# Kernel optimization log

Hardware: AMD Instinct MI355X
Metric: run time of the kernel (lower is better)

## Reference

```python
import jax, jax.numpy as jnp
import numpy as np

B, H, W, C = 64, 224, 224, 3
P = 16
DIM = 768
DEPTH = 12
NH, DH = 12, 64
FF = 3072
NPATCH = (H // P) * (W // P)   # 196
L = NPATCH + 1                 # 197 tokens (CLS + patches)
KEEP = int(L * (1.0 - 0.75))   # 49 unmasked tokens


def setup_inputs() -> dict:
    key = jax.random.key(0)
    ks = jax.random.split(key, 16)
    s = 0.02
    inp = {
        'inputs': jax.random.normal(ks[0], (B, H, W, C), jnp.float32),
        'conv_w': jax.random.normal(ks[1], (P, P, C, DIM), jnp.float32) * s,
        'ct':     jax.random.normal(ks[2], (1, 1, DIM), jnp.float32) * s,
        'pe':     jax.random.normal(ks[3], (1, L, DIM), jnp.float32) * s,
        'ln1_s': jnp.ones((DEPTH, DIM), jnp.float32),
        'ln1_b': jnp.zeros((DEPTH, DIM), jnp.float32),
        'qkv_w': jax.random.normal(ks[4], (DEPTH, DIM, 3 * NH * DH), jnp.float32) * s,
        'proj_w': jax.random.normal(ks[5], (DEPTH, NH * DH, DIM), jnp.float32) * s,
        'ln2_s': jnp.ones((DEPTH, DIM), jnp.float32),
        'ln2_b': jnp.zeros((DEPTH, DIM), jnp.float32),
        'w1': jax.random.normal(ks[6], (DEPTH, DIM, FF), jnp.float32) * s,
        'b1': jnp.zeros((DEPTH, FF), jnp.float32),
        'w2': jax.random.normal(ks[7], (DEPTH, FF, DIM), jnp.float32) * s,
        'b2': jnp.zeros((DEPTH, DIM), jnp.float32),
        # Faithful to original: permutation of arange(1, L+1); max value 197
        # is out-of-range and gets clamped by JAX gather, exactly as upstream.
        'mask_idx': jax.random.permutation(ks[8], jnp.arange(1, L + 1))[:KEEP].astype(jnp.int32),
    }
    return inp


def _layernorm(x, scale, bias, eps=1e-9):
    m = jnp.mean(x, axis=-1, keepdims=True)
    v = jnp.var(x, axis=-1, keepdims=True)
    return (x - m) * jax.lax.rsqrt(v + eps) * scale + bias


def _encoder(x, layer_params):
    # x: [B, KEEP, DIM]; layer_params leaves stacked on axis 0 (DEPTH)
    inv_sqrt_d = 1.0 / jnp.sqrt(jnp.float32(DH))

    def block(x, p):
        ln1s, ln1b, qw, pw, ln2s, ln2b, w1, b1, w2, b2 = p
        h = _layernorm(x, ln1s, ln1b)
        qkv = h @ qw                                   # [B, Lk, 3*NH*DH]
        q, k, v = jnp.split(qkv, 3, axis=-1)
        def heads(t):
            return t.reshape(x.shape[0], -1, NH, DH).transpose(0, 2, 1, 3)
        q, k, v = heads(q), heads(k), heads(v)         # [B, NH, Lk, DH]
        att = jax.nn.softmax(jnp.einsum('bhqd,bhkd->bhqk', q, k) * inv_sqrt_d)
        o = jnp.einsum('bhqk,bhkd->bhqd', att, v)
        o = o.transpose(0, 2, 1, 3).reshape(x.shape[0], -1, NH * DH) @ pw
        x = x + o
        h2 = _layernorm(x, ln2s, ln2b)
        x = x + (jax.nn.gelu(h2 @ w1 + b1) @ w2 + b2)
        return x, None

    x, _ = jax.lax.scan(block, x, layer_params)
    return x


def reference(inputs, conv_w, ct, pe, ln1_s, ln1_b, qkv_w, proj_w,
              ln2_s, ln2_b, w1, b1, w2, b2, mask_idx):
    # patch embed: stride-P conv, no bias
    out = jax.lax.conv_general_dilated(
        inputs, conv_w, window_strides=(P, P), padding='VALID',
        dimension_numbers=('NHWC', 'HWIO', 'NHWC'))      # [B, 14, 14, DIM]
    out = out.reshape(out.shape[0], -1, out.shape[3])     # [B, 196, DIM]
    out = jnp.concatenate((jnp.repeat(ct, out.shape[0], axis=0), out), axis=1)
    out = out + pe                                        # [B, 197, DIM]
    patches = out[:, mask_idx]                            # [B, 49, DIM]
    layer_params = (ln1_s, ln1_b, qkv_w, proj_w, ln2_s, ln2_b, w1, b1, w2, b2)
    return _encoder(patches, layer_params)
```

## Files before the change

### kernel.cpp

```cpp
#include <hip/hip_runtime.h>
#include <hip/hip_bf16.h>
#include <math.h>

#define DIMV   768
#define BATCH  64
#define KEEPT  49
#define MTOK   (BATCH*KEEPT)
#define NHEADS 12
#define DHEAD  64
#define FFV    3072
#define NDEPTH 12

typedef short short8 __attribute__((ext_vector_type(8)));
typedef float floatx4 __attribute__((ext_vector_type(4)));
typedef unsigned short ushort;
typedef unsigned short ushortx8 __attribute__((ext_vector_type(8)));

__device__ __forceinline__ ushort f2bf(float f) {
  __hip_bfloat16 h = __float2bfloat16(f);
  return *(ushort*)&h;
}

__device__ __forceinline__ void async_cp16(const void* g, void* l) {
  __builtin_amdgcn_global_load_lds((const __attribute__((address_space(1))) void*)g,
                                   (__attribute__((address_space(3))) void*)l,
                                   16, 0, 0);
}

__global__ __launch_bounds__(256) void gather_patches(
    const float* __restrict__ inp, const int* __restrict__ mask,
    __hip_bfloat16* __restrict__ apix)
{
  int gid = blockIdx.x * 256 + threadIdx.x;
  if (gid >= MTOK * DIMV) return;
  int r = gid / DIMV, k = gid - r * DIMV;
  int b = r / KEEPT, t = r - b * KEEPT;
  int j = mask[t];
  j = j < 0 ? 0 : (j > 196 ? 196 : j);
  float v = 0.f;
  if (j > 0) {
    int p  = j - 1, py = p / 14, px = p - py * 14;
    int ky = k / 48, rem = k - ky * 48, kx = rem / 3, c = rem - kx * 3;
    v = inp[(((b * 224) + py * 16 + ky) * 224 + px * 16 + kx) * 3 + c];
  }
  apix[gid] = __float2bfloat16(v);
}

__global__ __launch_bounds__(256) void layernorm_k(
    const float* __restrict__ x, const float* __restrict__ sc,
    const float* __restrict__ bi, __hip_bfloat16* __restrict__ out)
{
  __shared__ float red[8];
  int r = blockIdx.x;
  const float* xr = x + (size_t)r * DIMV;
  int t = threadIdx.x;
  float v[3];
  float s = 0.f, ss = 0.f;
#pragma unroll
  for (int i = 0; i < 3; i++) {
    float a = xr[t + i * 256];
    v[i] = a; s += a; ss += a * a;
  }
#pragma unroll
  for (int off = 32; off > 0; off >>= 1) {
    s  += __shfl_down(s,  off, 64);
    ss += __shfl_down(ss, off, 64);
  }
  int wave = t >> 6, lane = t & 63;
  if (lane == 0) { red[wave] = s; red[4 + wave] = ss; }
  __syncthreads();
  if (t == 0) {
    float a  = red[0] + red[1] + red[2] + red[3];
    float b2 = red[4] + red[5] + red[6] + red[7];
    float m  = a * (1.f / DIMV);
    float var = b2 * (1.f / DIMV) - m * m;
    red[0] = m;
    red[1] = rsqrtf(var + 1e-9f);
  }
  __syncthreads();
  float m = red[0], rs = red[1];
  __hip_bfloat16* outr = out + (size_t)r * DIMV;
#pragma unroll
  for (int i = 0; i < 3; i++) {
    int d = t + i * 256;
    outr[d] = __float2bfloat16((v[i] - m) * rs * sc[d] + bi[d]);
  }
}

__device__ __forceinline__ void transpose_tile64(
    const float* __restrict__ src, __hip_bfloat16* __restrict__ dst,
    int R, int C, int tr, int tcc)
{
  __shared__ float lds[64][65];
  const int tid = threadIdx.x;
  const int r0 = tr * 64, c0 = tcc * 64;
  const int lr = tid >> 4, lc4 = (tid & 15) * 4;
#pragma unroll
  for (int p = 0; p < 4; p++) {
    float4 v = *(const float4*)(src + (size_t)(r0 + p * 16 + lr) * C + c0 + lc4);
    lds[p * 16 + lr][lc4 + 0] = v.x;
    lds[p * 16 + lr][lc4 + 1] = v.y;
    lds[p * 16 + lr][lc4 + 2] = v.z;
    lds[p * 16 + lr][lc4 + 3] = v.w;
  }
  __syncthreads();
  const int c = tid >> 2, rc = (tid & 3) * 8;
  ushortx8 o0, o1;
#pragma unroll
  for (int j = 0; j < 8; j++) o0[j] = f2bf(lds[rc + j][c]);
#pragma unroll
  for (int j = 0; j < 8; j++) o1[j] = f2bf(lds[rc + 32 + j][c]);
  ushort* drow = (ushort*)dst + (size_t)(c0 + c) * R + r0;
  *(ushortx8*)(drow + rc)      = o0;
  *(ushortx8*)(drow + rc + 32) = o1;
}

__global__ __launch_bounds__(256) void transpose_one(
    const float* __restrict__ src, __hip_bfloat16* __restrict__ dst, int R, int C)
{
  int tc = C >> 6;
  transpose_tile64(src, dst, R, C, blockIdx.x / tc, blockIdx.x % tc);
}

#define QKV_TE  ((size_t)2304*768)
#define PROJ_TE ((size_t)768*768)
#define W1_TE   ((size_t)3072*768)
#define W2_TE   ((size_t)768*3072)
#define LSTRIDE (QKV_TE + PROJ_TE + W1_TE + W2_TE)

__global__ __launch_bounds__(256) void convert_weights(
    const float* __restrict__ qkv_w, const float* __restrict__ proj_w,
    const float* __restrict__ w1, const float* __restrict__ w2,
    __hip_bfloat16* __restrict__ dstBase, int layer0, size_t dstStride)
{
  int l = layer0 + blockIdx.y;
  __hip_bfloat16* d = dstBase + (size_t)blockIdx.y * dstStride;
  int tile = blockIdx.x;
  const float* src; __hip_bfloat16* dst; int R, C, t0;
  if (tile < 432)       { src = qkv_w  + (size_t)l*768*2304; dst = d;                          R=768;  C=2304; t0=tile; }
  else if (tile < 576)  { src = proj_w + (size_t)l*768*768;  dst = d + QKV_TE;                 R=768;  C=768;  t0=tile-432; }
  else if (tile < 1152) { src = w1     + (size_t)l*768*3072; dst = d + QKV_TE+PROJ_TE;         R=768;  C=3072; t0=tile-576; }
  else                  { src = w2     + (size_t)l*3072*768; dst = d + QKV_TE+PROJ_TE+W1_TE;   R=3072; C=768;  t0=tile-1152; }
  int tc = C >> 6;
  transpose_tile64(src, dst, R, C, t0 / tc, t0 % tc);
}

enum { EPI_NONE = 0, EPI_RESID = 1, EPI_BIAS_GELU = 2, EPI_BIAS_RESID = 3,
       EPI_EMBED = 4 };

template <int EPI, bool OUT_BF16>
__global__ __launch_bounds__(256) void gemm_mfma(
    const ushort* __restrict__ A, const ushort* __restrict__ Bt,
    const float* __restrict__ Cin, const float* __restrict__ bias,
    const float* __restrict__ pe, const int* __restrict__ mask,
    void* __restrict__ Cout, int M, int N, int K)
{
  __shared__ ushort As[2][128 * 64];
  __shared__ ushort Bs[2][64 * 64];

  const int tid  = threadIdx.x;
  const int wave = tid >> 6, lane = tid & 63;
  const int bm = blockIdx.y, bn = blockIdx.x;
  const int fr = lane & 15, fc = lane >> 4;

  floatx4 acc[2][4];
#pragma unroll
  for (int i = 0; i < 2; i++)
#pragma unroll
    for (int j = 0; j < 4; j++) { floatx4 z = {0.f,0.f,0.f,0.f}; acc[i][j] = z; }

  const int lrow   = lane >> 3;
  const int lchunk = ((lane & 7) ^ lrow) * 8;
  const ushort* aSrc[4];
#pragma unroll
  for (int i = 0; i < 4; i++) {
    int row = bm * 128 + wave * 32 + i * 8 + lrow;
    row = row < M - 1 ? row : M - 1;
    aSrc[i] = A + (size_t)row * K + lchunk;
  }
  const ushort* bSrc[2];
#pragma unroll
  for (int i = 0; i < 2; i++) {
    int row = bn * 64 + wave * 16 + i * 8 + lrow;
    bSrc[i] = Bt + (size_t)row * K + lchunk;
  }

  const int NT = K >> 6;

  {
    ushort* aD = &As[0][(wave * 32) * 64];
#pragma unroll
    for (int i = 0; i < 4; i++) async_cp16(aSrc[i], aD + i * 8 * 64);
    ushort* bD = &Bs[0][(wave * 16) * 64];
#pragma unroll
    for (int i = 0; i < 2; i++) async_cp16(bSrc[i], bD + i * 8 * 64);
  }
  asm volatile("s_waitcnt vmcnt(0)" ::: "memory");
  __builtin_amdgcn_s_barrier();
  __builtin_amdgcn_sched_barrier(0);

  int cur = 0;
  for (int t = 0; t < NT; t++) {
    if (t + 1 < NT) {
      const int k0 = (t + 1) << 6;
      ushort* aD = &As[cur ^ 1][(wave * 32) * 64];
#pragma unroll
      for (int i = 0; i < 4; i++) async_cp16(aSrc[i] + k0, aD + i * 8 * 64);
      ushort* bD = &Bs[cur ^ 1][(wave * 16) * 64];
#pragma unroll
      for (int i = 0; i < 2; i++) async_cp16(bSrc[i] + k0, bD + i * 8 * 64);
    }

    const ushort* Ab = As[cur];
    const ushort* Bb = Bs[cur];
    short8 af[2][2], bf[2][4];
#pragma unroll
    for (int kk = 0; kk < 2; kk++) {
      const int cbase = kk * 4 + fc;
      const int slot  = (cbase ^ (fr & 7)) * 8;
#pragma unroll
      for (int mt = 0; mt < 2; mt++)
        af[kk][mt] = *(const short8*)&Ab[(wave * 32 + mt * 16 + fr) * 64 + slot];
#pragma unroll
      for (int nt = 0; nt < 4; nt++)
        bf[kk][nt] = *(const short8*)&Bb[(nt * 16 + fr) * 64 + slot];
    }
    __builtin_amdgcn_s_setprio(1);
#pragma unroll
    for (int kk = 0; kk < 2; kk++)
#pragma unroll
      for (int mt = 0; mt < 2; mt++)
#pragma unroll
        for (int nt = 0; nt < 4; nt++)
          acc[mt][nt] = __builtin_amdgcn_mfma_f32_16x16x32_bf16(
              af[kk][mt], bf[kk][nt], acc[mt][nt], 0, 0, 0);
    __builtin_amdgcn_s_setprio(0);

    if (t + 1 < NT) {
      asm volatile("s_waitcnt vmcnt(0)" ::: "memory");
      __builtin_amdgcn_s_barrier();
      __builtin_amdgcn_sched_barrier(0);
    }
    cur ^= 1;
  }

  const int colb = bn * 64 + fr;
  const int rq   = fc * 4;
#pragma unroll
  for (int mt = 0; mt < 2; mt++) {
#pragma unroll
    for (int r = 0; r < 4; r++) {
      int row = bm * 128 + wave * 32 + mt * 16 + rq + r;
      if (row >= M) continue;
#pragma unroll
      for (int nt = 0; nt < 4; nt++) {
        int col = colb + nt * 16;
        float u = acc[mt][nt][r];
        if (EPI == EPI_BIAS_GELU || EPI == EPI_BIAS_RESID) u += bias[col];
        if (EPI == EPI_BIAS_GELU) {
          float t3 = u * u * u;
          u = 0.5f * u * (1.f + tanhf(0.7978845608028654f * (u + 0.044715f * t3)));
        }
        if (EPI == EPI_RESID || EPI == EPI_BIAS_RESID) u += Cin[(size_t)row * N + col];
        if (EPI == EPI_EMBED) {
          int t = row % KEEPT;
          int j = mask[t];
          j = j < 0 ? 0 : (j > 196 ? 196 : j);
          if (j == 0) u = bias[col];
          u += pe[(size_t)j * DIMV + col];
        }
        if (OUT_BF16)
          ((__hip_bfloat16*)Cout)[(size_t)row * N + col] = __float2bfloat16(u);
        else
          ((float*)Cout)[(size_t)row * N + col] = u;
      }
    }
  }
}

__global__ __launch_bounds__(256) void attn_mfma(
    const ushort* __restrict__ qkv, ushort* __restrict__ o)
{
  __shared__ ushort qA[64 * 72];
  __shared__ ushort kB[64 * 72];
  __shared__ ushort vT[64 * 72];
  __shared__ ushort pA[64 * 72];
  const int b = blockIdx.x, hh = blockIdx.y;
  const int tid = threadIdx.x;
  const int wave = tid >> 6, lane = tid & 63;
  const int fr = lane & 15, fc = lane >> 4;

  const ushort* base = qkv + (size_t)b * KEEPT * (3 * DIMV) + hh * 64;

#pragma unroll
  for (int it = 0; it < 2; it++) {
    int r  = it * 32 + wave * 8 + (lane >> 3);
    int cc = (lane & 7) * 8;
    short8 qv = {0,0,0,0,0,0,0,0};
    short8 kv = {0,0,0,0,0,0,0,0};
    if (r < KEEPT) {
      const ushort* row = base + (size_t)r * (3 * DIMV);
      qv = *(const short8*)(row + cc);
      kv = *(const short8*)(row + DIMV + cc);
    }
    *(short8*)&qA[r * 72 + cc] = qv;
    *(short8*)&kB[r * 72 + cc] = kv;
  }
  for (int r = wave; r < 64; r += 4) {
    ushort v = 0;
    if (r < KEEPT) v = base[(size_t)r * (3 * DIMV) + 2 * DIMV + lane];
    vT[lane * 72 + r] = v;
  }
  __syncthreads();

  const int q0 = wave * 16;
  floatx4 sacc[4];
#pragma unroll
  for (int nt = 0; nt < 4; nt++) { floatx4 z = {0.f,0.f,0.f,0.f}; sacc[nt] = z; }

#pragma unroll
  for (int kk = 0; kk < 2; kk++) {
    const int ch = kk * 32 + fc * 8;
    short8 af = *(const short8*)&qA[(q0 + fr) * 72 + ch];
#pragma unroll
    for (int nt = 0; nt < 4; nt++) {
      short8 bf = *(const short8*)&kB[(nt * 16 + fr) * 72 + ch];
      sacc[nt] = __builtin_amdgcn_mfma_f32_16x16x32_bf16(af, bf, sacc[nt], 0, 0, 0);
    }
  }

  float inv[4];
#pragma unroll
  for (int r = 0; r < 4; r++) {
    float mx = -1e30f;
#pragma unroll
    for (int nt = 0; nt < 4; nt++) {
      float s = sacc[nt][r] * 0.125f;
      if (nt == 3 && fr >= 1) s = -1e30f;
      sacc[nt][r] = s;
      mx = fmaxf(mx, s);
    }
    mx = fmaxf(mx, __shfl_xor(mx, 1, 64));
    mx = fmaxf(mx, __shfl_xor(mx, 2, 64));
    mx = fmaxf(mx, __shfl_xor(mx, 4, 64));
    mx = fmaxf(mx, __shfl_xor(mx, 8, 64));
    float sum = 0.f;
#pragma unroll
    for (int nt = 0; nt < 4; nt++) {
      float e = __expf(sacc[nt][r] - mx);
      sacc[nt][r] = e;
      sum += e;
    }
    sum += __shfl_xor(sum, 1, 64);
    sum += __shfl_xor(sum, 2, 64);
    sum += __shfl_xor(sum, 4, 64);
    sum += __shfl_xor(sum, 8, 64);
    inv[r] = 1.f / sum;
  }

#pragma unroll
  for (int r = 0; r < 4; r++)
#pragma unroll
    for (int nt = 0; nt < 4; nt++)
      pA[(q0 + fc * 4 + r) * 72 + nt * 16 + fr] = f2bf(sacc[nt][r]);
  __syncthreads();

  floatx4 oacc[4];
#pragma unroll
  for (int nt = 0; nt < 4; nt++) { floatx4 z = {0.f,0.f,0.f,0.f}; oacc[nt] = z; }

#pragma unroll
  for (int kk = 0; kk < 2; kk++) {
    const int ch = kk * 32 + fc * 8;
    short8 af = *(const short8*)&pA[(q0 + fr) * 72 + ch];
#pragma unroll
    for (int nt = 0; nt < 4; nt++) {
      short8 bf = *(const short8*)&vT[(nt * 16 + fr) * 72 + ch];
      oacc[nt] = __builtin_amdgcn_mfma_f32_16x16x32_bf16(af, bf, oacc[nt], 0, 0, 0);
    }
  }

  ushort* obase = o + (size_t)b * KEEPT * DIMV + hh * 64;
#pragma unroll
  for (int r = 0; r < 4; r++) {
    int q = q0 + fc * 4 + r;
    if (q < KEEPT) {
#pragma unroll
      for (int nt = 0; nt < 4; nt++)
        obase[(size_t)q * DIMV + nt * 16 + fr] = f2bf(oacc[nt][r] * inv[r]);
    }
  }
}

extern "C" void kernel_launch(void* const* d_in, const int* in_sizes, int n_in,
                              void* d_out, int out_size, void* d_ws, size_t ws_size,
                              hipStream_t stream)
{
  (void)in_sizes; (void)n_in; (void)out_size;
  const float* inputs = (const float*)d_in[0];
  const float* conv_w = (const float*)d_in[1];
  const float* ct     = (const float*)d_in[2];
  const float* pe     = (const float*)d_in[3];
  const float* ln1_s  = (const float*)d_in[4];
  const float* ln1_b  = (const float*)d_in[5];
  const float* qkv_w  = (const float*)d_in[6];
  const float* proj_w = (const float*)d_in[7];
  const float* ln2_s  = (const float*)d_in[8];
  const float* ln2_b  = (const float*)d_in[9];
  const float* w1     = (const float*)d_in[10];
  const float* b1     = (const float*)d_in[11];
  const float* w2     = (const float*)d_in[12];
  const float* b2     = (const float*)d_in[13];
  const int*   mask   = (const int*)d_in[14];
  float* out = (float*)d_out;

  char* wsb = (char*)d_ws;
  float*          x     = (float*)wsb;
  __hip_bfloat16* h     = (__hip_bfloat16*)(wsb + 9633792);
  __hip_bfloat16* big   = (__hip_bfloat16*)(wsb + 9633792 + 4816896);
  __hip_bfloat16* convT = (__hip_bfloat16*)(wsb + 9633792 + 4816896 + 19267584);
  __hip_bfloat16* wbuf  = (__hip_bfloat16*)(wsb + 9633792 + 4816896 + 19267584 + 1179648);
  const size_t base_bytes = 9633792ull + 4816896 + 19267584 + 1179648;
  const bool all_mode = ws_size >= base_bytes + 12ull * LSTRIDE * 2;

  __hip_bfloat16* apix = h;
  __hip_bfloat16* qkv  = big;
  __hip_bfloat16* g    = big;

  dim3 blk(256);
  const int nelem = MTOK * DIMV;
  const int nblk  = (nelem + 255) / 256;
  const int mg    = (MTOK + 127) / 128;

  transpose_one<<<144, blk, 0, stream>>>(conv_w, convT, 768, 768);
  if (all_mode)
    convert_weights<<<dim3(1728, 12), blk, 0, stream>>>(
        qkv_w, proj_w, w1, w2, wbuf, 0, LSTRIDE);

  gather_patches<<<nblk, blk, 0, stream>>>(inputs, mask, apix);
  gemm_mfma<EPI_EMBED, false><<<dim3(12, mg), blk, 0, stream>>>(
      (const ushort*)apix, (const ushort*)convT, nullptr, ct, pe, mask, x,
      MTOK, DIMV, DIMV);

  for (int l = 0; l < NDEPTH; l++) {
    __hip_bfloat16* wl = wbuf + (all_mode ? (size_t)l * LSTRIDE : 0);
    if (!all_mode)
      convert_weights<<<dim3(1728, 1), blk, 0, stream>>>(
          qkv_w, proj_w, w1, w2, wbuf, l, 0);
    const ushort* qkvT  = (const ushort*)wl;
    const ushort* projT = (const ushort*)(wl + QKV_TE);
    const ushort* w1T   = (const ushort*)(wl + QKV_TE + PROJ_TE);
    const ushort* w2T   = (const ushort*)(wl + QKV_TE + PROJ_TE + W1_TE);

    layernorm_k<<<MTOK, blk, 0, stream>>>(x, ln1_s + l * DIMV, ln1_b + l * DIMV, h);
    gemm_mfma<EPI_NONE, true><<<dim3(36, mg), blk, 0, stream>>>(
        (const ushort*)h, qkvT, nullptr, nullptr, nullptr, nullptr, qkv,
        MTOK, 3 * DIMV, DIMV);
    attn_mfma<<<dim3(BATCH, NHEADS), blk, 0, stream>>>(
        (const ushort*)qkv, (ushort*)h);
    gemm_mfma<EPI_RESID, false><<<dim3(12, mg), blk, 0, stream>>>(
        (const ushort*)h, projT, x, nullptr, nullptr, nullptr, x,
        MTOK, DIMV, DIMV);
    layernorm_k<<<MTOK, blk, 0, stream>>>(x, ln2_s + l * DIMV, ln2_b + l * DIMV, h);
    gemm_mfma<EPI_BIAS_GELU, true><<<dim3(48, mg), blk, 0, stream>>>(
        (const ushort*)h, w1T, nullptr, b1 + (size_t)l * FFV, nullptr, nullptr, g,
        MTOK, FFV, DIMV);
    float* dst = (l == NDEPTH - 1) ? out : x;
    gemm_mfma<EPI_BIAS_RESID, false><<<dim3(12, mg), blk, 0, stream>>>(
        (const ushort*)g, w2T, x, b2 + (size_t)l * DIMV, nullptr, nullptr, dst,
        MTOK, DIMV, FFV);
  }
}
```

Measured before the change: 2.297 ms.

## Add 128x128-tile GEMM for QKV/FFN1 and pipeline multi-tile weight conversion

Adds a 512-thread GEMM kernel with 128x128 output tiles. It is used for the QKV and FFN-up projections, which raises per-block data reuse and halves the number of blocks. The weight-conversion kernel now processes four 64x64 transpose tiles per block, using double-buffered LDS and register prefetch of the next tile to overlap global loads with the transpose. The trade-offs are fewer blocks in flight for the wide GEMMs, with possible occupancy or tail effects, and higher register and LDS pressure.

```diff
diff --git a/kernel.cpp b/kernel.cpp
--- a/kernel.cpp
+++ b/kernel.cpp
@@ -127,26 +127,101 @@
 #define W1_TE   ((size_t)3072*768)
 #define W2_TE   ((size_t)768*3072)
 #define LSTRIDE (QKV_TE + PROJ_TE + W1_TE + W2_TE)
+#define CW_TPG  4
+
+struct CwTile { const float* s; ushort* d; int R, C; };
 
 __global__ __launch_bounds__(256) void convert_weights(
     const float* __restrict__ qkv_w, const float* __restrict__ proj_w,
     const float* __restrict__ w1, const float* __restrict__ w2,
     __hip_bfloat16* __restrict__ dstBase, int layer0, size_t dstStride)
 {
-  int l = layer0 + blockIdx.y;
-  __hip_bfloat16* d = dstBase + (size_t)blockIdx.y * dstStride;
-  int tile = blockIdx.x;
-  const float* src; __hip_bfloat16* dst; int R, C, t0;
-  if (tile < 432)       { src = qkv_w  + (size_t)l*768*2304; dst = d;                          R=768;  C=2304; t0=tile; }
-  else if (tile < 576)  { src = proj_w + (size_t)l*768*768;  dst = d + QKV_TE;                 R=768;  C=768;  t0=tile-432; }
-  else if (tile < 1152) { src = w1     + (size_t)l*768*3072; dst = d + QKV_TE+PROJ_TE;         R=768;  C=3072; t0=tile-576; }
-  else                  { src = w2     + (size_t)l*3072*768; dst = d + QKV_TE+PROJ_TE+W1_TE;   R=3072; C=768;  t0=tile-1152; }
-  int tc = C >> 6;
-  transpose_tile64(src, dst, R, C, t0 / tc, t0 % tc);
+  __shared__ float lds[2][64][65];
+  const int l = layer0 + blockIdx.y;
+  __hip_bfloat16* dl = dstBase + (size_t)blockIdx.y * dstStride;
+  const int tid = threadIdx.x;
+  const int lr = tid >> 4, lc4 = (tid & 15) * 4;
+  const int oc = tid >> 2, orc = (tid & 3) * 8;
+
+  auto resolve = [&](int tile) -> CwTile {
+    const float* src; __hip_bfloat16* dst; int R, C, t0;
+    if (tile < 432)       { src = qkv_w  + (size_t)l*768*2304; dst = dl;                        R=768;  C=2304; t0=tile; }
+    else if (tile < 576)  { src = proj_w + (size_t)l*768*768;  dst = dl + QKV_TE;               R=768;  C=768;  t0=tile-432; }
+    else if (tile < 1152) { src = w1     + (size_t)l*768*3072; dst = dl + QKV_TE+PROJ_TE;       R=768;  C=3072; t0=tile-576; }
+    else                  { src = w2     + (size_t)l*3072*768; dst = dl + QKV_TE+PROJ_TE+W1_TE; R=3072; C=768;  t0=tile-1152; }
+    int tc = C >> 6, tr = t0 / tc, tcc = t0 % tc;
+    CwTile r;
+    r.s = src + (size_t)(tr * 64) * C + tcc * 64;
+    r.d = (ushort*)dst + (size_t)(tcc * 64) * R + tr * 64;
+    r.R = R; r.C = C;
+    return r;
+  };
+
+  const int tbase = blockIdx.x * CW_TPG;
+  CwTile cti = resolve(tbase);
+  float4 rv[4];
+#pragma unroll
+  for (int p = 0; p < 4; p++)
+    rv[p] = *(const float4*)(cti.s + (size_t)(p * 16 + lr) * cti.C + lc4);
+
+  int cur = 0;
+  for (int ti = 0; ti < CW_TPG; ti++) {
+#pragma unroll
+    for (int p = 0; p < 4; p++) {
+      lds[cur][p * 16 + lr][lc4 + 0] = rv[p].x;
+      lds[cur][p * 16 + lr][lc4 + 1] = rv[p].y;
+      lds[cur][p * 16 + lr][lc4 + 2] = rv[p].z;
+      lds[cur][p * 16 + lr][lc4 + 3] = rv[p].w;
+    }
+    __syncthreads();
+    CwTile nti;
+    if (ti + 1 < CW_TPG) {
+      nti = resolve(tbase + ti + 1);
+#pragma unroll
+      for (int p = 0; p < 4; p++)
+        rv[p] = *(const float4*)(nti.s + (size_t)(p * 16 + lr) * nti.C + lc4);
+    }
+    ushortx8 o0, o1;
+#pragma unroll
+    for (int j = 0; j < 8; j++) o0[j] = f2bf(lds[cur][orc + j][oc]);
+#pragma unroll
+    for (int j = 0; j < 8; j++) o1[j] = f2bf(lds[cur][orc + 32 + j][oc]);
+    ushort* drow = cti.d + (size_t)oc * cti.R;
+    *(ushortx8*)(drow + orc)      = o0;
+    *(ushortx8*)(drow + orc + 32) = o1;
+    if (ti + 1 < CW_TPG) cti = nti;
+    cur ^= 1;
+  }
 }
 
 enum { EPI_NONE = 0, EPI_RESID = 1, EPI_BIAS_GELU = 2, EPI_BIAS_RESID = 3,
        EPI_EMBED = 4 };
+
+template <int EPI, bool OUT_BF16>
+__device__ __forceinline__ void gemm_epilogue_elem(
+    float u, int row, int col, int N,
+    const float* __restrict__ Cin, const float* __restrict__ bias,
+    const float* __restrict__ pe, const int* __restrict__ mask,
+    void* __restrict__ Cout)
+{
+  if (EPI == EPI_BIAS_GELU || EPI == EPI_BIAS_RESID) u += bias[col];
+  if (EPI == EPI_BIAS_GELU) {
+    float t3 = u * u * u;
+    u = 0.5f * u * (1.f + tanhf(0.7978845608028654f * (u + 0.044715f * t3)));
+  }
+  if (EPI == EPI_RESID || EPI == EPI_BIAS_RESID) u += Cin[(size_t)row * N + col];
+  if (EPI == EPI_EMBED) {
+    int t = row % KEEPT;
+    int j = mask[t];
+    j = j < 0 ? 0 : (j > 196 ? 196 : j);
+    if (j == 0) u = bias[col];
+    u += pe[(size_t)j * DIMV + col];
+  }
+  if (OUT_BF16)
+    ((__hip_bfloat16*)Cout)[(size_t)row * N + col] = __float2bfloat16(u);
+  else
+    ((float*)Cout)[(size_t)row * N + col] = u;
+}
 
 template <int EPI, bool OUT_BF16>
 __global__ __launch_bounds__(256) void gemm_mfma(
@@ -186,7 +261,6 @@
   }
 
   const int NT = K >> 6;
-
   {
     ushort* aD = &As[0][(wave * 32) * 64];
 #pragma unroll
@@ -247,35 +321,127 @@
   const int colb = bn * 64 + fr;
   const int rq   = fc * 4;
 #pragma unroll
-  for (int mt = 0; mt < 2; mt++) {
+  for (int mt = 0; mt < 2; mt++)
 #pragma unroll
     for (int r = 0; r < 4; r++) {
       int row = bm * 128 + wave * 32 + mt * 16 + rq + r;
       if (row >= M) continue;
 #pragma unroll
-      for (int nt = 0; nt < 4; nt++) {
-        int col = colb + nt * 16;
-        float u = acc[mt][nt][r];
-        if (EPI == EPI_BIAS_GELU || EPI == EPI_BIAS_RESID) u += bias[col];
-        if (EPI == EPI_BIAS_GELU) {
-          float t3 = u * u * u;
-          u = 0.5f * u * (1.f + tanhf(0.7978845608028654f * (u + 0.044715f * t3)));
-        }
-        if (EPI == EPI_RESID || EPI == EPI_BIAS_RESID) u += Cin[(size_t)row * N + col];
-        if (EPI == EPI_EMBED) {
-          int t = row % KEEPT;
-          int j = mask[t];
-          j = j < 0 ? 0 : (j > 196 ? 196 : j);
-          if (j == 0) u = bias[col];
-          u += pe[(size_t)j * DIMV + col];
-        }
-        if (OUT_BF16)
-          ((__hip_bfloat16*)Cout)[(size_t)row * N + col] = __float2bfloat16(u);
-        else
-          ((float*)Cout)[(size_t)row * N + col] = u;
-      }
-    }
-  }
+      for (int nt = 0; nt < 4; nt++)
+        gemm_epilogue_elem<EPI, OUT_BF16>(acc[mt][nt][r], row, colb + nt * 16,
+                                          N, Cin, bias, pe, mask, Cout);
+    }
+}
+
+template <int EPI, bool OUT_BF16>
+__global__ __launch_bounds__(512) void gemm_big(
+    const ushort* __restrict__ A, const ushort* __restrict__ Bt,
+    const float* __restrict__ Cin, const float* __restrict__ bias,
+    const float* __restrict__ pe, const int* __restrict__ mask,
+    void* __restrict__ Cout, int M, int N, int K)
+{
+  __shared__ ushort As[2][128 * 64];
+  __shared__ ushort Bs[2][128 * 64];
+
+  const int tid  = threadIdx.x;
+  const int wave = tid >> 6, lane = tid & 63;
+  const int bm = blockIdx.y, bn = blockIdx.x;
+  const int fr = lane & 15, fc = lane >> 4;
+  const int wm0 = (wave >> 2) * 64, wn0 = (wave & 3) * 32;
+
+  floatx4 acc[4][2];
+#pragma unroll
+  for (int i = 0; i < 4; i++)
+#pragma unroll
+    for (int j = 0; j < 2; j++) { floatx4 z = {0.f,0.f,0.f,0.f}; acc[i][j] = z; }
+
+  const int lrow   = lane >> 3;
+  const int lchunk = ((lane & 7) ^ lrow) * 8;
+  const ushort* aSrc[2];
+#pragma unroll
+  for (int i = 0; i < 2; i++) {
+    int row = bm * 128 + wave * 16 + i * 8 + lrow;
+    row = row < M - 1 ? row : M - 1;
+    aSrc[i] = A + (size_t)row * K + lchunk;
+  }
+  const ushort* bSrc[2];
+#pragma unroll
+  for (int i = 0; i < 2; i++) {
+    int row = bn * 128 + wave * 16 + i * 8 + lrow;
+    bSrc[i] = Bt + (size_t)row * K + lchunk;
+  }
+
+  const int NT = K >> 6;
+  {
+    ushort* aD = &As[0][(wave * 16) * 64];
+#pragma unroll
+    for (int i = 0; i < 2; i++) async_cp16(aSrc[i], aD + i * 8 * 64);
+    ushort* bD = &Bs[0][(wave * 16) * 64];
+#pragma unroll
+    for (int i = 0; i < 2; i++) async_cp16(bSrc[i], bD + i * 8 * 64);
+  }
+  asm volatile("s_waitcnt vmcnt(0)" ::: "memory");
+  __builtin_amdgcn_s_barrier();
+  __builtin_amdgcn_sched_barrier(0);
+
+  int cur = 0;
+  for (int t = 0; t < NT; t++) {
+    if (t + 1 < NT) {
+      const int k0 = (t + 1) << 6;
+      ushort* aD = &As[cur ^ 1][(wave * 16) * 64];
+#pragma unroll
+      for (int i = 0; i < 2; i++) async_cp16(aSrc[i] + k0, aD + i * 8 * 64);
+      ushort* bD = &Bs[cur ^ 1][(wave * 16) * 64];
+#pragma unroll
+      for (int i = 0; i < 2; i++) async_cp16(bSrc[i] + k0, bD + i * 8 * 64);
+    }
+
+    const ushort* Ab = As[cur];
+    const ushort* Bb = Bs[cur];
+    short8 af[2][4], bf[2][2];
+#pragma unroll
+    for (int kk = 0; kk < 2; kk++) {
+      const int cbase = kk * 4 + fc;
+      const int slot  = (cbase ^ (fr & 7)) * 8;
+#pragma unroll
+      for (int mt = 0; mt < 4; mt++)
+        af[kk][mt] = *(const short8*)&Ab[(wm0 + mt * 16 + fr) * 64 + slot];
+#pragma unroll
+      for (int nt = 0; nt < 2; nt++)
+        bf[kk][nt] = *(const short8*)&Bb[(wn0 + nt * 16 + fr) * 64 + slot];
+    }
+    __builtin_amdgcn_s_setprio(1);
+#pragma unroll
+    for (int kk = 0; kk < 2; kk++)
+#pragma unroll
+      for (int mt = 0; mt < 4; mt++)
+#pragma unroll
+        for (int nt = 0; nt < 2; nt++)
+          acc[mt][nt] = __builtin_amdgcn_mfma_f32_16x16x32_bf16(
+              af[kk][mt], bf[kk][nt], acc[mt][nt], 0, 0, 0);
+    __builtin_amdgcn_s_setprio(0);
+
+    if (t + 1 < NT) {
+      asm volatile("s_waitcnt vmcnt(0)" ::: "memory");
+      __builtin_amdgcn_s_barrier();
+      __builtin_amdgcn_sched_barrier(0);
+    }
+    cur ^= 1;
+  }
+
+  const int colb = bn * 128 + wn0 + fr;
+  const int rq   = fc * 4;
+#pragma unroll
+  for (int mt = 0; mt < 4; mt++)
+#pragma unroll
+    for (int r = 0; r < 4; r++) {
+      int row = bm * 128 + wm0 + mt * 16 + rq + r;
+      if (row >= M) continue;
+#pragma unroll
+      for (int nt = 0; nt < 2; nt++)
+        gemm_epilogue_elem<EPI, OUT_BF16>(acc[mt][nt][r], row, colb + nt * 16,
+                                          N, Cin, bias, pe, mask, Cout);
+    }
 }
 
 __global__ __launch_bounds__(256) void attn_mfma(
@@ -428,13 +594,14 @@
   __hip_bfloat16* g    = big;
 
   dim3 blk(256);
+  dim3 blk2(512);
   const int nelem = MTOK * DIMV;
   const int nblk  = (nelem + 255) / 256;
   const int mg    = (MTOK + 127) / 128;
 
   transpose_one<<<144, blk, 0, stream>>>(conv_w, convT, 768, 768);
   if (all_mode)
-    convert_weights<<<dim3(1728, 12), blk, 0, stream>>>(
+    convert_weights<<<dim3(1728 / CW_TPG, 12), blk, 0, stream>>>(
         qkv_w, proj_w, w1, w2, wbuf, 0, LSTRIDE);
 
   gather_patches<<<nblk, blk, 0, stream>>>(inputs, mask, apix);
@@ -445,7 +612,7 @@
   for (int l = 0; l < NDEPTH; l++) {
     __hip_bfloat16* wl = wbuf + (all_mode ? (size_t)l * LSTRIDE : 0);
     if (!all_mode)
-      convert_weights<<<dim3(1728, 1), blk, 0, stream>>>(
+      convert_weights<<<dim3(1728 / CW_TPG, 1), blk, 0, stream>>>(
           qkv_w, proj_w, w1, w2, wbuf, l, 0);
     const ushort* qkvT  = (const ushort*)wl;
     const ushort* projT = (const ushort*)(wl + QKV_TE);
@@ -453,7 +620,7 @@
     const ushort* w2T   = (const ushort*)(wl + QKV_TE + PROJ_TE + W1_TE);
 
     layernorm_k<<<MTOK, blk, 0, stream>>>(x, ln1_s + l * DIMV, ln1_b + l * DIMV, h);
-    gemm_mfma<EPI_NONE, true><<<dim3(36, mg), blk, 0, stream>>>(
+    gemm_big<EPI_NONE, true><<<dim3(18, mg), blk2, 0, stream>>>(
         (const ushort*)h, qkvT, nullptr, nullptr, nullptr, nullptr, qkv,
         MTOK, 3 * DIMV, DIMV);
     attn_mfma<<<dim3(BATCH, NHEADS), blk, 0, stream>>>(
@@ -462,7 +629,7 @@
         (const ushort*)h, projT, x, nullptr, nullptr, nullptr, x,
         MTOK, DIMV, DIMV);
     layernorm_k<<<MTOK, blk, 0, stream>>>(x, ln2_s + l * DIMV, ln2_b + l * DIMV, h);
-    gemm_mfma<EPI_BIAS_GELU, true><<<dim3(48, mg), blk, 0, stream>>>(
+    gemm_big<EPI_BIAS_GELU, true><<<dim3(24, mg), blk2, 0, stream>>>(
         (const ushort*)h, w1T, nullptr, b1 + (size_t)l * FFV, nullptr, nullptr, g,
         MTOK, FFV, DIMV);
     float* dst = (l == NDEPTH - 1) ? out : x;
```

Measured after the change: 2.251 ms. 1.02x faster.
